# Kernel tuning notes

Measured on AMD Instinct MI355X. Metric: run time of the kernel, lower is better.

The kernel has to match this reference:

```python
import jax, jax.numpy as jnp
import numpy as np

WINDOW_SIZE = 11
WINDOW_SIGMA = 1.5
LOSS_WEIGHT = 1.0
PAD = WINDOW_SIZE // 2  # 5; applied to BOTH H and W as in the torch source


def _gaussian_window(channels):
    # Matches torch gaussian_window: 1-D gaussian reshaped to (1,1,1,ws),
    # repeated per channel -> OIHW kernel of shape (C, 1, 1, ws).
    coords = np.arange(WINDOW_SIZE, dtype=np.float32) - (WINDOW_SIZE // 2)
    g = np.exp(-coords ** 2 / (2.0 * WINDOW_SIGMA ** 2))
    g = g / g.sum()
    w = np.tile(g.reshape(1, 1, 1, WINDOW_SIZE), (channels, 1, 1, 1))
    return jnp.asarray(w)


def _dwconv(x, w, channels):
    # Depthwise conv, kernel (1, ws), zero padding 5 on both H and W
    # (faithful to F.conv2d(..., padding=5) with a (1,11) kernel, which
    # grows H by 10 -- intentional reproduction of the source behavior).
    return jax.lax.conv_general_dilated(
        x, w,
        window_strides=(1, 1),
        padding=((PAD, PAD), (PAD, PAD)),
        dimension_numbers=('NCHW', 'OIHW', 'NCHW'),
        feature_group_count=channels,
    )


def setup_inputs() -> dict:
    key = jax.random.key(0)
    k1, k2 = jax.random.split(key)
    shape = (16, 3, 512, 512)
    pred = jax.random.uniform(k1, shape, dtype=jnp.float32)
    target = jax.random.uniform(k2, shape, dtype=jnp.float32)
    return {"pred": pred, "target": target}


def reference(pred, target):
    channels = pred.shape[1]
    w = _gaussian_window(channels)
    conv = lambda x: _dwconv(x, w, channels)

    mu1 = conv(pred)              # (B, C, H+10, W)
    mu2 = conv(target)
    mu1_sq = mu1 * mu1
    mu2_sq = mu2 * mu2
    mu1_mu2 = mu1 * mu2

    sigma1_sq = conv(pred * pred) - mu1_sq
    sigma2_sq = conv(target * target) - mu2_sq
    sigma12 = conv(pred * target) - mu1_mu2

    C1 = 0.01 ** 2
    C2 = 0.03 ** 2
    ssim_map = ((2.0 * mu1_mu2 + C1) * (2.0 * sigma12 + C2)) / (
        (mu1_sq + mu2_sq + C1) * (sigma1_sq + sigma2_sq + C2))

    return LOSS_WEIGHT * (1.0 - ssim_map.mean())
```

## Files before the change

kernel.cpp:

```cpp
#include <hip/hip_runtime.h>
#include <hip/hip_fp16.h>
#include <cmath>

#define WS 11

struct GaussHalf {
    unsigned gA[WS];
    unsigned gS[WS];
    unsigned c11, c22;
};

__global__ __launch_bounds__(256) void ssim_row_kernel(
    const float* __restrict__ pred, const float* __restrict__ targ,
    GaussHalf gh, float* __restrict__ partials)
{
    const int t = threadIdx.x;
    const int lane = t & 63;
    const int wave = t >> 6;
    const int wave_id = blockIdx.x * 4 + wave;

    const long long off = (long long)wave_id * 512 + 8 * lane;
    const float* prow = pred + off;
    const float* trow = targ + off;

    float4 P0 = *reinterpret_cast<const float4*>(prow);
    float4 P1 = *reinterpret_cast<const float4*>(prow + 4);
    float4 Q0 = *reinterpret_cast<const float4*>(trow);
    float4 Q1 = *reinterpret_cast<const float4*>(trow + 4);

    const __half2 pm = __halves2half2(__float2half(1.f), __float2half(-1.f));
    const __half2 C11 = __builtin_bit_cast(__half2, gh.c11);
    const __half2 C22 = __builtin_bit_cast(__half2, gh.c22);

    float acc = 0.f;
    #pragma unroll
    for (int r = 0; r < 3; ++r) {
        float4 nP0, nP1, nQ0, nQ1;
        if (r < 2) {
            const float* pn = prow + (long long)(r + 1) * 8192 * 512;
            const float* tn = trow + (long long)(r + 1) * 8192 * 512;
            nP0 = *reinterpret_cast<const float4*>(pn);
            nP1 = *reinterpret_cast<const float4*>(pn + 4);
            nQ0 = *reinterpret_cast<const float4*>(tn);
            nQ1 = *reinterpret_cast<const float4*>(tn + 4);
        }

        __half2 w[18];
        {
            const float pv[8] = {P0.x, P0.y, P0.z, P0.w, P1.x, P1.y, P1.z, P1.w};
            const float qv[8] = {Q0.x, Q0.y, Q0.z, Q0.w, Q1.x, Q1.y, Q1.z, Q1.w};
            #pragma unroll
            for (int i = 0; i < 8; ++i)
                w[5 + i] = __floats2half2_rn(pv[i] + qv[i], pv[i] - qv[i]);
        }
        #pragma unroll
        for (int i = 0; i < 5; ++i) {
            const unsigned lu =
                __shfl_up(__builtin_bit_cast(unsigned, w[8 + i]), 1);
            const unsigned ru =
                __shfl_down(__builtin_bit_cast(unsigned, w[5 + i]), 1);
            w[i]      = __builtin_bit_cast(__half2, (lane == 0)  ? 0u : lu);
            w[13 + i] = __builtin_bit_cast(__half2, (lane == 63) ? 0u : ru);
        }
        __half2 s[18];
        #pragma unroll
        for (int i = 0; i < 18; ++i) s[i] = __hmul2(w[i], w[i]);

        #pragma unroll
        for (int px = 0; px < 8; ++px) {
            __half2 AB  = __builtin_bit_cast(__half2, 0u);
            __half2 SUV = __builtin_bit_cast(__half2, 0u);
            #pragma unroll
            for (int k = 0; k < WS; ++k) {
                AB  = __hfma2(__builtin_bit_cast(__half2, gh.gA[k]),
                              w[px + k], AB);
                SUV = __hfma2(__builtin_bit_cast(__half2, gh.gS[k]),
                              s[px + k], SUV);
            }
            const __half2 ab2  = __hmul2(AB, AB);
            const __half2 t2d2 = __hfma2(__lowhigh2highlow(ab2), pm, ab2);
            const __half2 tsds = __hfma2(__lowhigh2highlow(SUV), pm, SUV);
            const __half2 dn1  = __hfma2(t2d2, pm, C11);
            const __half2 dl   = __hsub2(tsds, t2d2);
            const __half2 dn2  = __hfma2(dl, pm, C22);
            const __half2 nd   = __hmul2(dn1, dn2);
            const float dd = __half2float(__low2half(nd));
            const float nn = __half2float(__high2half(nd));
            acc = fmaf(nn, __builtin_amdgcn_rcpf(dd), acc);
        }

        if (r < 2) { P0 = nP0; P1 = nP1; Q0 = nQ0; Q1 = nQ1; }
    }

    #pragma unroll
    for (int offr = 32; offr > 0; offr >>= 1)
        acc += __shfl_down(acc, offr);
    __shared__ float wsum[4];
    if (lane == 0) wsum[wave] = acc;
    __syncthreads();
    if (t == 0)
        partials[blockIdx.x] = wsum[0] + wsum[1] + wsum[2] + wsum[3];
}

__global__ __launch_bounds__(256) void ssim_final_kernel(
    const float* __restrict__ partials, float* __restrict__ out)
{
    const int t = threadIdx.x;
    double d = 0.0;
    #pragma unroll
    for (int i = 0; i < 8; ++i)
        d += (double)partials[t + 256 * i];
    #pragma unroll
    for (int offr = 32; offr > 0; offr >>= 1)
        d += __shfl_down(d, offr);
    __shared__ double wsumd[4];
    const int lane = t & 63, wave = t >> 6;
    if (lane == 0) wsumd[wave] = d;
    __syncthreads();
    if (t == 0) {
        const double s = wsumd[0] + wsumd[1] + wsumd[2] + wsumd[3] + 245760.0;
        out[0] = (float)(1.0 - s / 12828672.0);
    }
}

static unsigned packh2(float x) {
    const __half h = __float2half(x);
    unsigned short hb;
    __builtin_memcpy(&hb, &h, 2);
    return ((unsigned)hb << 16) | hb;
}

extern "C" void kernel_launch(void* const* d_in, const int* in_sizes, int n_in,
                              void* d_out, int out_size, void* d_ws, size_t ws_size,
                              hipStream_t stream) {
    const float* pred = (const float*)d_in[0];
    const float* targ = (const float*)d_in[1];
    float* out = (float*)d_out;
    float* partials = (float*)d_ws;

    GaussHalf gh;
    double graw[WS], s = 0.0;
    for (int i = 0; i < WS; ++i) {
        const double c = (double)(i - WS / 2);
        graw[i] = exp(-c * c / (2.0 * 1.5 * 1.5));
        s += graw[i];
    }
    for (int i = 0; i < WS; ++i) {
        const double g = graw[i] / s;
        gh.gA[i] = packh2((float)(g * 0.70710678118654752));
        gh.gS[i] = packh2((float)(g * 0.5));
    }
    gh.c11 = packh2(0.0001f);
    gh.c22 = packh2(0.0009f);

    ssim_row_kernel<<<2048, 256, 0, stream>>>(pred, targ, gh, partials);
    ssim_final_kernel<<<1, 256, 0, stream>>>(partials, out);
}
```

Baseline: 25.56 us.

## Assign one row per wave, triple grid size, drop block-level reduction

Each wave now processes a single row instead of three rows strided across the tensor, so the grid grows from 2048 to 6144 blocks, and launch bounds request 8 blocks per CU. Wave sums go straight to the partials buffer, which removes the shared-memory block reduction and its barrier. The final kernel grows to 1024 threads to sum the 24576 wave partials. The cost is losing the software prefetch of the next row and tripling the number of partials the final single-block kernel must read.

New measurement: 24.89 us. -2.6%, faster.

```diff
diff --git a/kernel.cpp b/kernel.cpp
--- a/kernel.cpp
+++ b/kernel.cpp
@@ -10,115 +10,98 @@
     unsigned c11, c22;
 };
 
-__global__ __launch_bounds__(256) void ssim_row_kernel(
+__global__ __launch_bounds__(256, 8) void ssim_row_kernel(
     const float* __restrict__ pred, const float* __restrict__ targ,
     GaussHalf gh, float* __restrict__ partials)
 {
     const int t = threadIdx.x;
     const int lane = t & 63;
-    const int wave = t >> 6;
-    const int wave_id = blockIdx.x * 4 + wave;
+    const int wid = (blockIdx.x << 2) | (t >> 6);
 
-    const long long off = (long long)wave_id * 512 + 8 * lane;
+    const long long off = (long long)wid * 512 + 8 * lane;
     const float* prow = pred + off;
     const float* trow = targ + off;
 
-    float4 P0 = *reinterpret_cast<const float4*>(prow);
-    float4 P1 = *reinterpret_cast<const float4*>(prow + 4);
-    float4 Q0 = *reinterpret_cast<const float4*>(trow);
-    float4 Q1 = *reinterpret_cast<const float4*>(trow + 4);
+    const float4 P0 = *reinterpret_cast<const float4*>(prow);
+    const float4 P1 = *reinterpret_cast<const float4*>(prow + 4);
+    const float4 Q0 = *reinterpret_cast<const float4*>(trow);
+    const float4 Q1 = *reinterpret_cast<const float4*>(trow + 4);
 
     const __half2 pm = __halves2half2(__float2half(1.f), __float2half(-1.f));
     const __half2 C11 = __builtin_bit_cast(__half2, gh.c11);
     const __half2 C22 = __builtin_bit_cast(__half2, gh.c22);
 
+    __half2 w[18];
+    {
+        const float pv[8] = {P0.x, P0.y, P0.z, P0.w, P1.x, P1.y, P1.z, P1.w};
+        const float qv[8] = {Q0.x, Q0.y, Q0.z, Q0.w, Q1.x, Q1.y, Q1.z, Q1.w};
+        #pragma unroll
+        for (int i = 0; i < 8; ++i)
+            w[5 + i] = __floats2half2_rn(pv[i] + qv[i], pv[i] - qv[i]);
+    }
+    #pragma unroll
+    for (int i = 0; i < 5; ++i) {
+        const unsigned lu =
+            __shfl_up(__builtin_bit_cast(unsigned, w[8 + i]), 1);
+        const unsigned ru =
+            __shfl_down(__builtin_bit_cast(unsigned, w[5 + i]), 1);
+        w[i]      = __builtin_bit_cast(__half2, (lane == 0)  ? 0u : lu);
+        w[13 + i] = __builtin_bit_cast(__half2, (lane == 63) ? 0u : ru);
+    }
+    __half2 s[18];
+    #pragma unroll
+    for (int i = 0; i < 18; ++i) s[i] = __hmul2(w[i], w[i]);
+
     float acc = 0.f;
     #pragma unroll
-    for (int r = 0; r < 3; ++r) {
-        float4 nP0, nP1, nQ0, nQ1;
-        if (r < 2) {
-            const float* pn = prow + (long long)(r + 1) * 8192 * 512;
-            const float* tn = trow + (long long)(r + 1) * 8192 * 512;
-            nP0 = *reinterpret_cast<const float4*>(pn);
-            nP1 = *reinterpret_cast<const float4*>(pn + 4);
-            nQ0 = *reinterpret_cast<const float4*>(tn);
-            nQ1 = *reinterpret_cast<const float4*>(tn + 4);
+    for (int px = 0; px < 8; ++px) {
+        __half2 AB  = __builtin_bit_cast(__half2, 0u);
+        __half2 SUV = __builtin_bit_cast(__half2, 0u);
+        #pragma unroll
+        for (int k = 0; k < WS; ++k) {
+            AB  = __hfma2(__builtin_bit_cast(__half2, gh.gA[k]),
+                          w[px + k], AB);
+            SUV = __hfma2(__builtin_bit_cast(__half2, gh.gS[k]),
+                          s[px + k], SUV);
         }
-
-        __half2 w[18];
-        {
-            const float pv[8] = {P0.x, P0.y, P0.z, P0.w, P1.x, P1.y, P1.z, P1.w};
-            const float qv[8] = {Q0.x, Q0.y, Q0.z, Q0.w, Q1.x, Q1.y, Q1.z, Q1.w};
-            #pragma unroll
-            for (int i = 0; i < 8; ++i)
-                w[5 + i] = __floats2half2_rn(pv[i] + qv[i], pv[i] - qv[i]);
-        }
-        #pragma unroll
-        for (int i = 0; i < 5; ++i) {
-            const unsigned lu =
-                __shfl_up(__builtin_bit_cast(unsigned, w[8 + i]), 1);
-            const unsigned ru =
-                __shfl_down(__builtin_bit_cast(unsigned, w[5 + i]), 1);
-            w[i]      = __builtin_bit_cast(__half2, (lane == 0)  ? 0u : lu);
-            w[13 + i] = __builtin_bit_cast(__half2, (lane == 63) ? 0u : ru);
-        }
-        __half2 s[18];
-        #pragma unroll
-        for (int i = 0; i < 18; ++i) s[i] = __hmul2(w[i], w[i]);
-
-        #pragma unroll
-        for (int px = 0; px < 8; ++px) {
-            __half2 AB  = __builtin_bit_cast(__half2, 0u);
-            __half2 SUV = __builtin_bit_cast(__half2, 0u);
-            #pragma unroll
-            for (int k = 0; k < WS; ++k) {
-                AB  = __hfma2(__builtin_bit_cast(__half2, gh.gA[k]),
-                              w[px + k], AB);
-                SUV = __hfma2(__builtin_bit_cast(__half2, gh.gS[k]),
-                              s[px + k], SUV);
-            }
-            const __half2 ab2  = __hmul2(AB, AB);
-            const __half2 t2d2 = __hfma2(__lowhigh2highlow(ab2), pm, ab2);
-            const __half2 tsds = __hfma2(__lowhigh2highlow(SUV), pm, SUV);
-            const __half2 dn1  = __hfma2(t2d2, pm, C11);
-            const __half2 dl   = __hsub2(tsds, t2d2);
-            const __half2 dn2  = __hfma2(dl, pm, C22);
-            const __half2 nd   = __hmul2(dn1, dn2);
-            const float dd = __half2float(__low2half(nd));
-            const float nn = __half2float(__high2half(nd));
-            acc = fmaf(nn, __builtin_amdgcn_rcpf(dd), acc);
-        }
-
-        if (r < 2) { P0 = nP0; P1 = nP1; Q0 = nQ0; Q1 = nQ1; }
+        const __half2 ab2  = __hmul2(AB, AB);
+        const __half2 t2d2 = __hfma2(__lowhigh2highlow(ab2), pm, ab2);
+        const __half2 tsds = __hfma2(__lowhigh2highlow(SUV), pm, SUV);
+        const __half2 dn1  = __hfma2(t2d2, pm, C11);
+        const __half2 dl   = __hsub2(tsds, t2d2);
+        const __half2 dn2  = __hfma2(dl, pm, C22);
+        const __half2 nd   = __hmul2(dn1, dn2);
+        const float dd = __half2float(__low2half(nd));
+        const float nn = __half2float(__high2half(nd));
+        acc = fmaf(nn, __builtin_amdgcn_rcpf(dd), acc);
     }
 
     #pragma unroll
     for (int offr = 32; offr > 0; offr >>= 1)
         acc += __shfl_down(acc, offr);
-    __shared__ float wsum[4];
-    if (lane == 0) wsum[wave] = acc;
-    __syncthreads();
-    if (t == 0)
-        partials[blockIdx.x] = wsum[0] + wsum[1] + wsum[2] + wsum[3];
+    if (lane == 0)
+        partials[wid] = acc;
 }
 
-__global__ __launch_bounds__(256) void ssim_final_kernel(
+__global__ __launch_bounds__(1024) void ssim_final_kernel(
     const float* __restrict__ partials, float* __restrict__ out)
 {
     const int t = threadIdx.x;
     double d = 0.0;
     #pragma unroll
-    for (int i = 0; i < 8; ++i)
-        d += (double)partials[t + 256 * i];
+    for (int i = 0; i < 24; ++i)
+        d += (double)partials[t + 1024 * i];
     #pragma unroll
     for (int offr = 32; offr > 0; offr >>= 1)
         d += __shfl_down(d, offr);
-    __shared__ double wsumd[4];
+    __shared__ double wsumd[16];
     const int lane = t & 63, wave = t >> 6;
     if (lane == 0) wsumd[wave] = d;
     __syncthreads();
     if (t == 0) {
-        const double s = wsumd[0] + wsumd[1] + wsumd[2] + wsumd[3] + 245760.0;
+        double s = 245760.0;
+        #pragma unroll
+        for (int i = 0; i < 16; ++i) s += wsumd[i];
         out[0] = (float)(1.0 - s / 12828672.0);
     }
 }
@@ -153,6 +136,6 @@
     gh.c11 = packh2(0.0001f);
     gh.c22 = packh2(0.0009f);
 
-    ssim_row_kernel<<<2048, 256, 0, stream>>>(pred, targ, gh, partials);
-    ssim_final_kernel<<<1, 256, 0, stream>>>(partials, out);
+    ssim_row_kernel<<<6144, 256, 0, stream>>>(pred, targ, gh, partials);
+    ssim_final_kernel<<<1, 1024, 0, stream>>>(partials, out);
 }
```
